# Kernel optimization log

Hardware: AMD Instinct MI355X
Metric: run time of the kernel (lower is better)

The kernel has to match this reference:

```python
import jax, jax.numpy as jnp
import numpy as np


def setup_inputs() -> dict:
    key = jax.random.key(0)
    k1, k2, k3, k4 = jax.random.split(key, 4)
    I, Q, P, S, N = 512000, 128, 1, 8, 4000
    x = jax.random.normal(k1, (I, Q), dtype=jnp.float32)
    beta_u = jax.random.normal(k2, (Q, P, S), dtype=jnp.float32)
    beta_z = jax.random.normal(k3, (Q, P, S), dtype=jnp.float32)
    i = jnp.sort(jax.random.randint(k4, (I,), 0, N, dtype=jnp.int64))
    return {"x": x, "beta_u": beta_u, "beta_z": beta_z, "i": i, "n_bags": N}


def _scatter_softmax(u, seg, num_segments):
    # numerically stable softmax over variable-size segments (bags)
    seg_max = jax.ops.segment_max(u, seg, num_segments=num_segments)  # [N,P,S]
    e = jnp.exp(u - seg_max[seg])                                     # [I,P,S]
    denom = jax.ops.segment_sum(e, seg, num_segments=num_segments)    # [N,P,S]
    return e / denom[seg]


def reference(x, beta_u, beta_z, i, n_bags):
    # b = rms of beta_z over latent dim -> [1,P,S]; eta = normalized beta_z
    b = jnp.sqrt(jnp.mean(beta_z ** 2, axis=0, keepdims=True))
    eta = beta_z / b
    # gather -> per-instance projections -> scatter softmax -> segment pooling
    u = jnp.einsum('iq,qps->ips', x, beta_u)      # [I,P,S]
    w = _scatter_softmax(u, i, n_bags)            # [I,P,S]
    z = jnp.einsum('iq,qps->ips', x, eta)         # [I,P,S]
    xmil = jax.ops.segment_sum(w * z, i, num_segments=n_bags)  # [N,P,S]
    # normalize across bags (torch .std is unbiased, ddof=1), rescale by b
    mean = jnp.mean(xmil, axis=0)
    std = jnp.std(xmil, axis=0, ddof=1)
    return b * (xmil - mean) / std
```

## Files before the change

kernel.cpp:

```cpp
#include <hip/hip_runtime.h>
#include <hip/hip_bf16.h>


#define QDIM 128
#define C8 8

typedef __attribute__((ext_vector_type(8))) short s8v;
typedef __attribute__((ext_vector_type(4))) float f4v;

__device__ __forceinline__ unsigned short bf16_rne(float f) {
    union { float f; unsigned u; } v; v.f = f;
    unsigned b = v.u;
    b += 0x7FFFu + ((b >> 16) & 1u);
    return (unsigned short)(b >> 16);
}
__device__ __forceinline__ float bf16f(unsigned short h) {
    union { unsigned u; float f; } v; v.u = ((unsigned)h) << 16;
    return v.f;
}

__global__ void mixmil_bounds(const int* __restrict__ seg, int I, int N,
                              int* __restrict__ bs)
{
    int k = blockIdx.x * blockDim.x + threadIdx.x;
    if (k > I) return;
    int a    = (k < I) ? seg[k]     : N;
    int prev = (k > 0) ? seg[k - 1] : -1;
    for (int j = prev + 1; j <= a; ++j) bs[j] = k;
}

__global__ __launch_bounds__(256) void mixmil_fused(
    const float* __restrict__ x,
    const float* __restrict__ bu,
    const float* __restrict__ bz,
    const int*   __restrict__ bs,
    int I, int N,
    float* __restrict__ xmil)
{
    __shared__ float XT[64 * QDIM];
    __shared__ float UZ[64 * 17];

    const int t    = threadIdx.x;
    const int lane = t & 63;
    const int wv   = t >> 6;

    const int b4    = blockIdx.x * 4;
    const int start = bs[b4];
    const int end   = bs[(b4 + 4 < N) ? (b4 + 4) : N];
    const int mybag = b4 + wv;
    const int lo = bs[mybag];
    const int hi = bs[mybag + 1];

    const int bn  = lane & 15;
    const int bkg = lane >> 4;
    s8v BH[4], BL[4];
    const float* wcol = (bn < 8) ? (bu + bn) : (bz + (bn - 8));
#pragma unroll
    for (int kc = 0; kc < 4; ++kc) {
#pragma unroll
        for (int j = 0; j < 8; ++j) {
            const int k = kc * 32 + bkg * 8 + j;
            const float w = wcol[(size_t)k * 8];
            const unsigned short h = bf16_rne(w);
            BH[kc][j] = (short)h;
            BL[kc][j] = (short)bf16_rne(w - bf16f(h));
        }
    }

    float lL[8], aA[8];
#pragma unroll
    for (int c = 0; c < 8; ++c) { lL[c] = 0.f; aA[c] = 0.f; }

    const int am  = lane & 15;
    const int akg = lane >> 4;

    for (int r0 = start; r0 < end; r0 += 64) {
#pragma unroll
        for (int i = 0; i < 8; ++i) {
            const int f  = i * 256 + t;
            const int r  = f >> 5;
            const int c4 = f & 31;
            int grow = r0 + r;
            if (grow >= end) grow = end - 1;
            const float4 v = *(const float4*)(x + (size_t)grow * QDIM + 4 * (size_t)c4);
            *(float4*)&XT[r * QDIM + 4 * (c4 ^ (r & 7))] = v;
        }
        __syncthreads();

        {
            const int r  = wv * 16 + am;
            const int sw = r & 7;
            f4v acc = {0.f, 0.f, 0.f, 0.f};
#pragma unroll
            for (int kc = 0; kc < 4; ++kc) {
                const int c4a = kc * 8 + akg * 2;
                const float4 xa = *(const float4*)&XT[r * QDIM + 4 * ((c4a    ) ^ sw)];
                const float4 xb = *(const float4*)&XT[r * QDIM + 4 * ((c4a + 1) ^ sw)];
                const float xs[8] = {xa.x, xa.y, xa.z, xa.w, xb.x, xb.y, xb.z, xb.w};
                s8v AH, AL;
#pragma unroll
                for (int j = 0; j < 8; ++j) {
                    const unsigned short h = bf16_rne(xs[j]);
                    AH[j] = (short)h;
                    AL[j] = (short)bf16_rne(xs[j] - bf16f(h));
                }
                acc = __builtin_amdgcn_mfma_f32_16x16x32_bf16(AH, BH[kc], acc, 0, 0, 0);
                acc = __builtin_amdgcn_mfma_f32_16x16x32_bf16(AH, BL[kc], acc, 0, 0, 0);
                acc = __builtin_amdgcn_mfma_f32_16x16x32_bf16(AL, BH[kc], acc, 0, 0, 0);
            }
            const int ccol  = lane & 15;
            const int crow0 = (lane >> 4) * 4;
#pragma unroll
            for (int i = 0; i < 4; ++i)
                UZ[(wv * 16 + crow0 + i) * 17 + ccol] = acc[i];
        }
        __syncthreads();

        {
            const int a0  = (lo > r0) ? lo : r0;
            const int bnd = (hi < r0 + 64) ? hi : (r0 + 64);
            const int k = a0 + lane;
            if (k < bnd) {
                const float* uzr = &UZ[(k - r0) * 17];
#pragma unroll
                for (int c = 0; c < 8; ++c) {
                    const float e = __expf(uzr[c]);
                    lL[c] += e;
                    aA[c] = fmaf(e, uzr[8 + c], aA[c]);
                }
            }
        }
        __syncthreads();
    }

    for (int off = 32; off; off >>= 1) {
#pragma unroll
        for (int c = 0; c < 8; ++c) {
            lL[c] += __shfl_xor(lL[c], off);
            aA[c] += __shfl_xor(aA[c], off);
        }
    }

    if (lane == 0) {
        const bool nonempty = hi > lo;
#pragma unroll
        for (int c = 0; c < 8; ++c)
            xmil[(size_t)mybag * 8 + c] = nonempty ? (aA[c] / lL[c]) : 0.f;
    }
}

__global__ __launch_bounds__(256) void mixmil_statsout(
    const float* __restrict__ xmil,
    const float* __restrict__ bz,
    int N, int total,
    float* __restrict__ out)
{
    double s[8], qq[8];
    float t2[8];
#pragma unroll
    for (int c = 0; c < 8; ++c) { s[c] = 0.0; qq[c] = 0.0; t2[c] = 0.f; }

    for (int r = threadIdx.x; r < N; r += 256) {
        const float* row = xmil + (size_t)r * 8;
#pragma unroll
        for (int c = 0; c < 8; ++c) {
            float v = row[c];
            s[c] += v;
            qq[c] += (double)v * (double)v;
        }
    }
    for (int r = threadIdx.x; r < QDIM; r += 256) {
        const float* row = bz + (size_t)r * 8;
#pragma unroll
        for (int c = 0; c < 8; ++c) { float v = row[c]; t2[c] = fmaf(v, v, t2[c]); }
    }

    for (int off = 32; off; off >>= 1) {
#pragma unroll
        for (int c = 0; c < 8; ++c) {
            s[c]  += __shfl_xor(s[c], off);
            qq[c] += __shfl_xor(qq[c], off);
            t2[c] += __shfl_xor(t2[c], off);
        }
    }

    __shared__ double S[4][8], QQ[4][8];
    __shared__ float T2[4][8];
    __shared__ float fb[8], fm[8], fr[8];
    const int w = threadIdx.x >> 6;
    if ((threadIdx.x & 63) == 0) {
#pragma unroll
        for (int c = 0; c < 8; ++c) { S[w][c] = s[c]; QQ[w][c] = qq[c]; T2[w][c] = t2[c]; }
    }
    __syncthreads();
    if (threadIdx.x < 8) {
        const int c = threadIdx.x;
        double ss = S[0][c] + S[1][c] + S[2][c] + S[3][c];
        double qs = QQ[0][c] + QQ[1][c] + QQ[2][c] + QQ[3][c];
        float  tt = T2[0][c] + T2[1][c] + T2[2][c] + T2[3][c];
        double mean = ss / (double)N;
        double var  = (qs - ss * ss / (double)N) / (double)(N - 1);
        fb[c] = sqrtf(tt / (float)QDIM);
        fm[c] = (float)mean;
        fr[c] = (float)(1.0 / sqrt(var));
    }
    __syncthreads();

    const int e = blockIdx.x * 256 + threadIdx.x;
    if (e < total) {
        const int c = e & 7;
        out[e] = fb[c] * (xmil[e] - fm[c]) * fr[c];
    }
}

extern "C" void kernel_launch(void* const* d_in, const int* in_sizes, int n_in,
                              void* d_out, int out_size, void* d_ws, size_t ws_size,
                              hipStream_t stream) {
    const float* x  = (const float*)d_in[0];
    const float* bu = (const float*)d_in[1];
    const float* bz = (const float*)d_in[2];
    const int*   sg = (const int*)d_in[3];

    const int I = in_sizes[0] / QDIM;
    const int N = out_size / C8;

    float* xmil = (float*)d_ws;
    int*   bs   = (int*)(xmil + (size_t)N * C8);

    mixmil_bounds<<<(I + 256) / 256, 256, 0, stream>>>(sg, I, N, bs);

    mixmil_fused<<<(N + 3) / 4, 256, 0, stream>>>(x, bu, bz, bs, I, N, xmil);

    const int total = N * C8;
    mixmil_statsout<<<(total + 255) / 256, 256, 0, stream>>>(
        xmil, bz, N, total, (float*)d_out);
}
```

Measured before the change: 65.91 us.

## Give each wave its own bag with double-buffered direct-to-LDS loads

Each wavefront now processes its own bag independently in 16-row tiles, instead of the block sharing 64-row tiles across 4 bags. Tiles are staged with global_load_lds into a per-wave double buffer, and vmcnt waits overlap the next load with the MFMA compute. This removes the block-wide __syncthreads and the shared UZ round trip. The softmax accumulation is now done in registers via lane shuffles. Small bags waste more of each 16-row tile, and the hand-written waitcnt counts must match the number of loads issued per stage.

```diff
diff --git a/kernel.cpp b/kernel.cpp
--- a/kernel.cpp
+++ b/kernel.cpp
@@ -37,17 +37,14 @@
     int I, int N,
     float* __restrict__ xmil)
 {
-    __shared__ float XT[64 * QDIM];
-    __shared__ float UZ[64 * 17];
+    __shared__ float XT[4 * 2 * 2048];
 
     const int t    = threadIdx.x;
     const int lane = t & 63;
     const int wv   = t >> 6;
 
-    const int b4    = blockIdx.x * 4;
-    const int start = bs[b4];
-    const int end   = bs[(b4 + 4 < N) ? (b4 + 4) : N];
-    const int mybag = b4 + wv;
+    const int mybag = blockIdx.x * 4 + wv;
+    if (mybag >= N) return;
     const int lo = bs[mybag];
     const int hi = bs[mybag + 1];
 
@@ -67,86 +64,92 @@
         }
     }
 
-    float lL[8], aA[8];
-#pragma unroll
-    for (int c = 0; c < 8; ++c) { lL[c] = 0.f; aA[c] = 0.f; }
+    float* const myXT = &XT[wv * 4096];
+    const int rl   = lane >> 5;
+    const int c4l  = lane & 31;
+
+    const int nt = (hi - lo + 15) >> 4;
+
+#define STAGE(J, SEL)                                                          \
+    {                                                                          \
+        const int base_ = lo + (J) * 16;                                       \
+        _Pragma("unroll")                                                      \
+        for (int i = 0; i < 8; ++i) {                                          \
+            const int r_ = i * 2 + rl;                                         \
+            int grow_ = base_ + r_;                                            \
+            if (grow_ >= hi) grow_ = hi - 1;                                   \
+            const int c4g_ = c4l ^ (r_ & 7);                                   \
+            const float* src_ = x + (size_t)grow_ * QDIM + 4 * (size_t)c4g_;   \
+            __builtin_amdgcn_global_load_lds(                                  \
+                (const __attribute__((address_space(1))) unsigned int*)src_,   \
+                (__attribute__((address_space(3))) unsigned int*)              \
+                    &myXT[(SEL) * 2048 + i * 256],                             \
+                16, 0, 0);                                                     \
+        }                                                                      \
+    }
+
+    float lsum = 0.f, asum = 0.f;
 
     const int am  = lane & 15;
     const int akg = lane >> 4;
-
-    for (int r0 = start; r0 < end; r0 += 64) {
-#pragma unroll
-        for (int i = 0; i < 8; ++i) {
-            const int f  = i * 256 + t;
-            const int r  = f >> 5;
-            const int c4 = f & 31;
-            int grow = r0 + r;
-            if (grow >= end) grow = end - 1;
-            const float4 v = *(const float4*)(x + (size_t)grow * QDIM + 4 * (size_t)c4);
-            *(float4*)&XT[r * QDIM + 4 * (c4 ^ (r & 7))] = v;
-        }
-        __syncthreads();
-
-        {
-            const int r  = wv * 16 + am;
-            const int sw = r & 7;
-            f4v acc = {0.f, 0.f, 0.f, 0.f};
-#pragma unroll
-            for (int kc = 0; kc < 4; ++kc) {
-                const int c4a = kc * 8 + akg * 2;
-                const float4 xa = *(const float4*)&XT[r * QDIM + 4 * ((c4a    ) ^ sw)];
-                const float4 xb = *(const float4*)&XT[r * QDIM + 4 * ((c4a + 1) ^ sw)];
-                const float xs[8] = {xa.x, xa.y, xa.z, xa.w, xb.x, xb.y, xb.z, xb.w};
-                s8v AH, AL;
-#pragma unroll
-                for (int j = 0; j < 8; ++j) {
-                    const unsigned short h = bf16_rne(xs[j]);
-                    AH[j] = (short)h;
-                    AL[j] = (short)bf16_rne(xs[j] - bf16f(h));
-                }
-                acc = __builtin_amdgcn_mfma_f32_16x16x32_bf16(AH, BH[kc], acc, 0, 0, 0);
-                acc = __builtin_amdgcn_mfma_f32_16x16x32_bf16(AH, BL[kc], acc, 0, 0, 0);
-                acc = __builtin_amdgcn_mfma_f32_16x16x32_bf16(AL, BH[kc], acc, 0, 0, 0);
+    const int sw  = am & 7;
+
+    if (nt > 0) STAGE(0, 0);
+
+    for (int j = 0; j < nt; ++j) {
+        const int sel = j & 1;
+        if (j + 1 < nt) {
+            STAGE(j + 1, sel ^ 1);
+            asm volatile("s_waitcnt vmcnt(8)" ::: "memory");
+        } else {
+            asm volatile("s_waitcnt vmcnt(0)" ::: "memory");
+        }
+        __builtin_amdgcn_sched_barrier(0);
+
+        const float* buf = &myXT[sel * 2048];
+
+        f4v acc = {0.f, 0.f, 0.f, 0.f};
+#pragma unroll
+        for (int kc = 0; kc < 4; ++kc) {
+            const int c4a = kc * 8 + akg * 2;
+            const float4 xa = *(const float4*)&buf[am * QDIM + 4 * ((c4a    ) ^ sw)];
+            const float4 xb = *(const float4*)&buf[am * QDIM + 4 * ((c4a + 1) ^ sw)];
+            const float xs[8] = {xa.x, xa.y, xa.z, xa.w, xb.x, xb.y, xb.z, xb.w};
+            s8v AH, AL;
+#pragma unroll
+            for (int jj = 0; jj < 8; ++jj) {
+                const unsigned short h = bf16_rne(xs[jj]);
+                AH[jj] = (short)h;
+                AL[jj] = (short)bf16_rne(xs[jj] - bf16f(h));
             }
-            const int ccol  = lane & 15;
-            const int crow0 = (lane >> 4) * 4;
-#pragma unroll
-            for (int i = 0; i < 4; ++i)
-                UZ[(wv * 16 + crow0 + i) * 17 + ccol] = acc[i];
-        }
-        __syncthreads();
-
-        {
-            const int a0  = (lo > r0) ? lo : r0;
-            const int bnd = (hi < r0 + 64) ? hi : (r0 + 64);
-            const int k = a0 + lane;
-            if (k < bnd) {
-                const float* uzr = &UZ[(k - r0) * 17];
-#pragma unroll
-                for (int c = 0; c < 8; ++c) {
-                    const float e = __expf(uzr[c]);
-                    lL[c] += e;
-                    aA[c] = fmaf(e, uzr[8 + c], aA[c]);
-                }
+            acc = __builtin_amdgcn_mfma_f32_16x16x32_bf16(AH, BH[kc], acc, 0, 0, 0);
+            acc = __builtin_amdgcn_mfma_f32_16x16x32_bf16(AH, BL[kc], acc, 0, 0, 0);
+            acc = __builtin_amdgcn_mfma_f32_16x16x32_bf16(AL, BH[kc], acc, 0, 0, 0);
+        }
+
+        const int base = lo + j * 16;
+        const int r0   = (lane >> 4) * 4;
+#pragma unroll
+        for (int i = 0; i < 4; ++i) {
+            const float uv = acc[i];
+            const float zv = __shfl_xor(uv, 8);
+            const bool valid = (base + r0 + i) < hi;
+            if ((lane & 15) < 8 && valid) {
+                const float e = __expf(uv);
+                lsum += e;
+                asum = fmaf(e, zv, asum);
             }
         }
-        __syncthreads();
-    }
-
-    for (int off = 32; off; off >>= 1) {
-#pragma unroll
-        for (int c = 0; c < 8; ++c) {
-            lL[c] += __shfl_xor(lL[c], off);
-            aA[c] += __shfl_xor(aA[c], off);
-        }
-    }
-
-    if (lane == 0) {
-        const bool nonempty = hi > lo;
-#pragma unroll
-        for (int c = 0; c < 8; ++c)
-            xmil[(size_t)mybag * 8 + c] = nonempty ? (aA[c] / lL[c]) : 0.f;
-    }
+    }
+
+    lsum += __shfl_xor(lsum, 16);
+    asum += __shfl_xor(asum, 16);
+    lsum += __shfl_xor(lsum, 32);
+    asum += __shfl_xor(asum, 32);
+
+    if (lane < 8)
+        xmil[(size_t)mybag * 8 + lane] = (hi > lo) ? (asum / lsum) : 0.f;
+#undef STAGE
 }
 
 __global__ __launch_bounds__(256) void mixmil_statsout(
```

Result: no change. 66.40 us (+0.7%).
